# Performance work log

Hardware: AMD Instinct MI355X
Metric: run time of the kernel (lower is better)

## Reference

```python
import jax, jax.numpy as jnp
import numpy as np

B, C1, C2, H, W = 4, 96, 96, 40, 40
DE, DI, R, N, K, E, TOPK = 192, 192, 6, 16, 4, 4, 2
EPS_BN = 1e-5
EPS_LN = 1e-5


def conv1x1(x, w):
    # x: (B,C,H,W), w: (O,C)
    return jnp.einsum('bchw,oc->bohw', x, w)


def dwconv3(x, w, b):
    # depthwise 3x3, w: (C,1,3,3)
    C = x.shape[1]
    y = jax.lax.conv_general_dilated(x, w, (1, 1), 'SAME',
                                     dimension_numbers=('NCHW', 'OIHW', 'NCHW'),
                                     feature_group_count=C)
    return y + b[None, :, None, None]


def bn_eval(x, g, b):
    # BatchNorm2d in eval mode with running_mean=0, running_var=1
    s = g / jnp.sqrt(1.0 + EPS_BN)
    return x * s[None, :, None, None] + b[None, :, None, None]


def layernorm(x, g, b):
    m = x.mean(-1, keepdims=True)
    xc = x - m
    v = (xc * xc).mean(-1, keepdims=True)
    return xc / jnp.sqrt(v + EPS_LN) * g + b


def gelu(x):
    return jax.nn.gelu(x, approximate=False)


def selective_scan(xs, dts, As, Bs, Cs):
    # xs, dts: (B,K,D,L); As: (K,D,N); Bs, Cs: (B,K,N,L)
    Bb, Kk, Dd, L = xs.shape
    Nn = As.shape[-1]
    xs_l = jnp.moveaxis(xs, -1, 0)   # (L,B,K,D)
    dts_l = jnp.moveaxis(dts, -1, 0)
    Bs_l = jnp.moveaxis(Bs, -1, 0)   # (L,B,K,N)
    Cs_l = jnp.moveaxis(Cs, -1, 0)
    h0 = jnp.zeros((Bb, Kk, Dd, Nn), xs.dtype)

    def step(h, inp):
        x_t, dt_t, B_t, C_t = inp
        dA = jnp.exp(dt_t[..., None] * As)                  # (B,K,D,N)
        h = h * dA + (dt_t * x_t)[..., None] * B_t[:, :, None, :]
        y = jnp.einsum('bkdn,bkn->bkd', h, C_t)
        return h, y

    _, ys = jax.lax.scan(step, h0, (xs_l, dts_l, Bs_l, Cs_l))
    return jnp.moveaxis(ys, 0, -1)   # (B,K,D,L)


def ss2d(x, in_proj_w, conv_w, conv_b, x_proj_w, dt_w, dt_b, A_logs, Ds,
         onorm_g, onorm_b, out_proj_w):
    # x: (B, C2, H, W)
    xz = conv1x1(x, in_proj_w)                      # (B, 2*DE, H, W)
    xx, z = jnp.split(xz, 2, axis=1)
    z1 = gelu(z)
    xx = gelu(dwconv3(xx, conv_w, conv_b))          # (B, DE, H, W)

    Bb, Dd, Hh, Ww = xx.shape
    L = Hh * Ww
    x_hw = xx.reshape(Bb, Dd, L)
    x_wh = xx.transpose(0, 1, 3, 2).reshape(Bb, Dd, L)
    xs = jnp.stack([x_hw, x_wh, x_hw[..., ::-1], x_wh[..., ::-1]], axis=1)  # (B,K,D,L)

    x_dbl = jnp.einsum('bkdl,kcd->bkcl', xs, x_proj_w)
    dts_r = x_dbl[:, :, :R]
    Bs = x_dbl[:, :, R:R + N]
    Cs = x_dbl[:, :, R + N:]
    dts = jnp.einsum('bkrl,kdr->bkdl', dts_r, dt_w)
    dts = jax.nn.softplus(dts + dt_b[None, :, :, None])
    As = -jnp.exp(A_logs.reshape(K, Dd, N))

    ys = selective_scan(xs, dts, As, Bs, Cs)
    ys = ys + Ds.reshape(K, Dd)[None, :, :, None] * xs

    # CrossMerge
    y = ys[:, 0] + ys[:, 2, :, ::-1]
    y_wh = ys[:, 1] + ys[:, 3, :, ::-1]
    y = y + y_wh.reshape(Bb, Dd, Ww, Hh).transpose(0, 1, 3, 2).reshape(Bb, Dd, L)

    y = layernorm(y.transpose(0, 2, 1), onorm_g, onorm_b)   # (B,L,D)
    y = y.reshape(Bb, Hh, Ww, Dd).transpose(0, 3, 1, 2)     # (B,D,H,W)
    y = y * z1
    return conv1x1(y, out_proj_w)


def moe(x, router_w, router_b, dw_w, dw_b, pw_w, pw_b):
    Bb = x.shape[0]
    g = x.mean(axis=(2, 3))                                 # (B,C)
    logits = g @ router_w.T + router_b
    prob = jax.nn.softmax(logits / 2.0, axis=-1)
    tp, ti = jax.lax.top_k(prob, TOPK)
    tp = tp / tp.sum(-1, keepdims=True)
    wmat = jnp.zeros((Bb, E), x.dtype).at[jnp.arange(Bb)[:, None], ti].add(tp)
    out = jnp.zeros_like(x)
    for e in range(E):
        h = gelu(dwconv3(x, dw_w[e], dw_b[e]))
        h = conv1x1(h, pw_w[e]) + pw_b[e][None, :, None, None]
        out = out + wmat[:, e][:, None, None, None] * h
    return out


def _forward(x, proj_w, bn0_g, bn0_b, ls_fc1_w, ls_fc1_b, ls_bn_g, ls_bn_b,
             ls_fc2_w, ls_fc2_b, ls_fc3_w, ls_fc3_b, n1_g, n1_b,
             in_proj_w, conv_w, conv_b, x_proj_w, dt_w, dt_b, A_logs, Ds,
             onorm_g, onorm_b, out_proj_w, n2_g, n2_b,
             router_w, router_b, moe_dw_w, moe_dw_b, moe_pw_w, moe_pw_b):
    x = jax.nn.silu(bn_eval(conv1x1(x, proj_w), bn0_g, bn0_b))
    res1 = x
    # LSBlock
    h = dwconv3(x, ls_fc1_w, ls_fc1_b)
    h = bn_eval(h, ls_bn_g, ls_bn_b)
    h = conv1x1(h, ls_fc2_w) + ls_fc2_b[None, :, None, None]
    h = gelu(h)
    h = conv1x1(h, ls_fc3_w) + ls_fc3_b[None, :, None, None]
    x1 = x + h
    x1 = ss2d(bn_eval(x1, n1_g, n1_b), in_proj_w, conv_w, conv_b, x_proj_w,
              dt_w, dt_b, A_logs, Ds, onorm_g, onorm_b, out_proj_w)
    x = res1 + x1
    x2 = moe(bn_eval(x, n2_g, n2_b), router_w, router_b,
             moe_dw_w, moe_dw_b, moe_pw_w, moe_pw_b)
    return x + x2


def setup_inputs() -> dict:
    key = jax.random.key(0)
    ks = jax.random.split(key, 16)
    rn = lambda k, shape, s: jax.random.normal(k, shape, jnp.float32) * s
    ones = lambda *s: jnp.ones(s, jnp.float32)
    zeros = lambda *s: jnp.zeros(s, jnp.float32)
    return {
        'x': jax.random.normal(ks[0], (B, C1, H, W), jnp.float32),
        'proj_w': rn(ks[1], (C2, C1), 0.1),
        'bn0_g': ones(C2), 'bn0_b': zeros(C2),
        'ls_fc1_w': rn(ks[2], (C2, 1, 3, 3), 0.2), 'ls_fc1_b': zeros(C2),
        'ls_bn_g': ones(C2), 'ls_bn_b': zeros(C2),
        'ls_fc2_w': rn(ks[3], (C2, C2), 0.1), 'ls_fc2_b': zeros(C2),
        'ls_fc3_w': rn(ks[4], (C2, C2), 0.1), 'ls_fc3_b': zeros(C2),
        'n1_g': ones(C2), 'n1_b': zeros(C2),
        'in_proj_w': rn(ks[5], (2 * DE, C2), 0.1),
        'conv_w': rn(ks[6], (DE, 1, 3, 3), 0.2), 'conv_b': zeros(DE),
        'x_proj_w': rn(ks[7], (K, R + 2 * N, DI), 0.1),
        'dt_w': rn(ks[8], (K, DI, R), 0.3),
        'dt_b': rn(ks[9], (K, DI), 0.5),
        'A_logs': rn(ks[10], (K * DI, N), 0.5),
        'Ds': ones(K * DI),
        'onorm_g': ones(DI), 'onorm_b': zeros(DI),
        'out_proj_w': rn(ks[11], (C2, DE), 0.1),
        'n2_g': ones(C2), 'n2_b': zeros(C2),
        'router_w': rn(ks[12], (E, C2), 0.1), 'router_b': zeros(E),
        'moe_dw_w': rn(ks[13], (E, C2, 1, 3, 3), 0.2), 'moe_dw_b': zeros(E, C2),
        'moe_pw_w': rn(ks[14], (E, C2, C2), 0.1), 'moe_pw_b': zeros(E, C2),
    }


def reference(x, proj_w, bn0_g, bn0_b, ls_fc1_w, ls_fc1_b, ls_bn_g, ls_bn_b,
              ls_fc2_w, ls_fc2_b, ls_fc3_w, ls_fc3_b, n1_g, n1_b,
              in_proj_w, conv_w, conv_b, x_proj_w, dt_w, dt_b, A_logs, Ds,
              onorm_g, onorm_b, out_proj_w, n2_g, n2_b,
              router_w, router_b, moe_dw_w, moe_dw_b, moe_pw_w, moe_pw_b):
    return _forward(x, proj_w, bn0_g, bn0_b, ls_fc1_w, ls_fc1_b, ls_bn_g, ls_bn_b,
                    ls_fc2_w, ls_fc2_b, ls_fc3_w, ls_fc3_b, n1_g, n1_b,
                    in_proj_w, conv_w, conv_b, x_proj_w, dt_w, dt_b, A_logs, Ds,
                    onorm_g, onorm_b, out_proj_w, n2_g, n2_b,
                    router_w, router_b, moe_dw_w, moe_dw_b, moe_pw_w, moe_pw_b)
```

## Files before the change

kernel.cpp:

```cpp
#include <hip/hip_runtime.h>
#include <hip/hip_bf16.h>
#include <math.h>

#define BB 4
#define CC 96
#define LL 1600
#define DD 192
#define KK 4
#define RR 6
#define NN 16
#define EE 4
#define NCH 40
#define CLEN 40

typedef __hip_bfloat16 bf16;

__device__ __forceinline__ float geluf(float x){ return 0.5f*x*(1.0f+erff(x*0.70710678118654752440f)); }
__device__ __forceinline__ float softplusf(float x){ return (x>20.0f)? x : __logf(1.0f+__expf(x)); }
#define BNS rsqrtf(1.0f + 1e-5f)
#define LOG2E 1.44269504088896340736f

__device__ __forceinline__ int xpos(int k, int l){
  if (k==0) return l;
  if (k==2) return LL-1-l;
  int t = (k==1)? l : (LL-1-l);
  return (t%40)*40 + t/40;
}

struct P33 { const void* p[33]; };
#define NTOT 790660
__device__ const int g_cum[34] = {
  0, 614400, 623616, 623712, 623808, 624672, 624768, 624864, 624960,
  634176, 634272, 643488, 643584, 643680, 643776, 680640, 682368, 682560,
  711744, 716352, 717120, 729408, 730176, 730368, 730560, 748992, 749088,
  749184, 749568, 749572, 753028, 753412, 790276, 790660
};

__global__ void k_convert(P33 ps, float* cv){
  bool f32 = (((const unsigned*)ps.p[21])[0] == 0x3F800000u);
  int idx = blockIdx.x*256 + threadIdx.x;
  if (idx >= NTOT) return;
  int lo=0, hi=33;
  while (lo+1<hi){ int mid=(lo+hi)>>1; if (idx >= g_cum[mid]) lo=mid; else hi=mid; }
  int local = idx - g_cum[lo];
  float v = f32 ? ((const float*)ps.p[lo])[local]
                : __bfloat162float(((const bf16*)ps.p[lo])[local]);
  cv[idx] = v;
}

__global__ void k_proj(const float* x, const float* w, const float* g, const float* b_, float* out){
  __shared__ float lx[96*64];
  int bid = blockIdx.x;
  int ot = bid%3, lt = (bid/3)%25, b = bid/75;
  int l0 = lt*64, ob = ot*32;
  const float* inb = x + b*CC*LL;
  for (int i=threadIdx.x; i<96*64; i+=256) lx[i] = inb[(i>>6)*LL + l0 + (i&63)];
  __syncthreads();
  int oq = threadIdx.x>>5, lq = threadIdx.x&31;
  float acc[4][2] = {};
  #pragma unroll 4
  for (int c=0;c<96;c++){
    float x0 = lx[c*64+lq], x1 = lx[c*64+lq+32];
    #pragma unroll
    for (int jo=0;jo<4;jo++){
      float wv = w[(ob+oq+8*jo)*CC + c];
      acc[jo][0] += wv*x0; acc[jo][1] += wv*x1;
    }
  }
  #pragma unroll
  for (int jo=0;jo<4;jo++){
    int o = ob+oq+8*jo;
    float sc = g[o]*BNS, bb = b_[o];
    #pragma unroll
    for (int jl=0;jl<2;jl++){
      float v = acc[jo][jl]*sc + bb;
      out[(b*CC+o)*LL + l0+lq+32*jl] = v/(1.0f+__expf(-v));
    }
  }
}

__global__ void k_fc_gelu(const float* in, const float* w, const float* bias, float* out){
  __shared__ float lx[96*64];
  int bid = blockIdx.x;
  int ot = bid%3, lt = (bid/3)%25, b = bid/75;
  int l0 = lt*64, ob = ot*32;
  const float* inb = in + b*CC*LL;
  for (int i=threadIdx.x; i<96*64; i+=256) lx[i] = inb[(i>>6)*LL + l0 + (i&63)];
  __syncthreads();
  int oq = threadIdx.x>>5, lq = threadIdx.x&31;
  float acc[4][2] = {};
  #pragma unroll 4
  for (int c=0;c<96;c++){
    float x0 = lx[c*64+lq], x1 = lx[c*64+lq+32];
    #pragma unroll
    for (int jo=0;jo<4;jo++){
      float wv = w[(ob+oq+8*jo)*CC + c];
      acc[jo][0] += wv*x0; acc[jo][1] += wv*x1;
    }
  }
  #pragma unroll
  for (int jo=0;jo<4;jo++){
    int o = ob+oq+8*jo;
    float bb = bias[o];
    out[(b*CC+o)*LL + l0+lq]    = geluf(acc[jo][0]+bb);
    out[(b*CC+o)*LL + l0+lq+32] = geluf(acc[jo][1]+bb);
  }
}

__global__ void k_fc_res_bn(const float* in, const float* w, const float* bias, const float* res,
                            const float* g, const float* b_, float* out){
  __shared__ float lx[96*64];
  int bid = blockIdx.x;
  int ot = bid%3, lt = (bid/3)%25, b = bid/75;
  int l0 = lt*64, ob = ot*32;
  const float* inb = in + b*CC*LL;
  for (int i=threadIdx.x; i<96*64; i+=256) lx[i] = inb[(i>>6)*LL + l0 + (i&63)];
  __syncthreads();
  int oq = threadIdx.x>>5, lq = threadIdx.x&31;
  float acc[4][2] = {};
  #pragma unroll 4
  for (int c=0;c<96;c++){
    float x0 = lx[c*64+lq], x1 = lx[c*64+lq+32];
    #pragma unroll
    for (int jo=0;jo<4;jo++){
      float wv = w[(ob+oq+8*jo)*CC + c];
      acc[jo][0] += wv*x0; acc[jo][1] += wv*x1;
    }
  }
  #pragma unroll
  for (int jo=0;jo<4;jo++){
    int o = ob+oq+8*jo;
    float bb = bias[o], sc = g[o]*BNS, b2 = b_[o];
    #pragma unroll
    for (int jl=0;jl<2;jl++){
      int pos = (b*CC+o)*LL + l0+lq+32*jl;
      float v = acc[jo][jl] + bb + res[pos];
      out[pos] = v*sc + b2;
    }
  }
}

__global__ void k_inproj(const float* in, const float* w, float* xxp, float* z1){
  __shared__ float lx[96*64];
  int bid = blockIdx.x;
  int ot = bid%12, lt = (bid/12)%25, b = bid/300;
  int l0 = lt*64, ob = ot*32;
  const float* inb = in + b*CC*LL;
  for (int i=threadIdx.x; i<96*64; i+=256) lx[i] = inb[(i>>6)*LL + l0 + (i&63)];
  __syncthreads();
  int oq = threadIdx.x>>5, lq = threadIdx.x&31;
  float acc[4][2] = {};
  #pragma unroll 4
  for (int c=0;c<96;c++){
    float x0 = lx[c*64+lq], x1 = lx[c*64+lq+32];
    #pragma unroll
    for (int jo=0;jo<4;jo++){
      float wv = w[(ob+oq+8*jo)*CC + c];
      acc[jo][0] += wv*x0; acc[jo][1] += wv*x1;
    }
  }
  if (ot < 6){
    #pragma unroll
    for (int jo=0;jo<4;jo++){
      int oc = ob+oq+8*jo;
      xxp[(b*DD+oc)*LL + l0+lq]    = acc[jo][0];
      xxp[(b*DD+oc)*LL + l0+lq+32] = acc[jo][1];
    }
  } else {
    __syncthreads();
    #pragma unroll
    for (int jo=0;jo<4;jo++){
      int oo = oq+8*jo;
      lx[lq*33 + oo]      = geluf(acc[jo][0]);
      lx[(lq+32)*33 + oo] = geluf(acc[jo][1]);
    }
    __syncthreads();
    int zb = ob - 192;
    for (int i=threadIdx.x; i<64*32; i+=256){
      int u = i>>5, oo = i&31;
      z1[(b*LL + l0+u)*DD + zb + oo] = lx[u*33 + oo];
    }
  }
}

__global__ void k_ssconv(const float* in, const float* w, const float* bias, float* out){
  int idx = blockIdx.x*256 + threadIdx.x;
  if (idx >= BB*DD*LL) return;
  int l = idx%LL, d = (idx/LL)%DD, b = idx/(LL*DD);
  int y = l/40, x0 = l%40;
  const float* ip = in + (b*DD+d)*LL;
  float acc = 0.f;
  #pragma unroll
  for (int ky=0;ky<3;ky++){
    int yy = y+ky-1; if (yy<0||yy>=40) continue;
    #pragma unroll
    for (int kx=0;kx<3;kx++){
      int xx = x0+kx-1; if (xx<0||xx>=40) continue;
      acc += w[d*9+ky*3+kx] * ip[yy*40+xx];
    }
  }
  out[idx] = geluf(acc + bias[d]);
}

__global__ void k_dwbn(const float* in, const float* w, const float* bias, const float* g, const float* b_, float* out){
  int idx = blockIdx.x*256 + threadIdx.x;
  if (idx >= BB*CC*LL) return;
  int l = idx%LL, c = (idx/LL)%CC, b = idx/(LL*CC);
  int y = l/40, x0 = l%40;
  const float* ip = in + (b*CC+c)*LL;
  float acc = 0.f;
  #pragma unroll
  for (int ky=0;ky<3;ky++){
    int yy = y+ky-1; if (yy<0||yy>=40) continue;
    #pragma unroll
    for (int kx=0;kx<3;kx++){
      int xx = x0+kx-1; if (xx<0||xx>=40) continue;
      acc += w[c*9+ky*3+kx] * ip[yy*40+xx];
    }
  }
  acc += bias[c];
  out[idx] = acc*(g[c]*BNS) + b_[c];
}

__global__ void k_xs(const float* xx, float* xs){
  __shared__ float t[32][33];
  int bid = blockIdx.x;
  int lt = bid % 50, dt = (bid/50)%6, b = bid/300;
  int l0 = lt*32, d0 = dt*32;
  int tx = threadIdx.x & 31, ty = threadIdx.x >> 5;
  #pragma unroll
  for (int j=0;j<4;j++){
    int dd = ty + 8*j;
    t[dd][tx] = xx[(b*DD + d0+dd)*LL + l0 + tx];
  }
  __syncthreads();
  #pragma unroll
  for (int j=0;j<4;j++){
    int ll = ty + 8*j;
    int l = l0 + ll;
    float v = t[tx][ll];
    int lw = (l%40)*40 + l/40;
    xs[((b*2+0)*LL + l )*DD + d0 + tx] = v;
    xs[((b*2+1)*LL + lw)*DD + d0 + tx] = v;
  }
}

__global__ void k_xw(const float* xx, float* xw1, float* Y){
  __shared__ float sm[40*41];
  int bd = blockIdx.x;
  const float* ip = xx + bd*LL;
  float* op = xw1 + bd*LL;
  for (int i=threadIdx.x; i<LL; i+=256) sm[(i/40)*41 + (i%40)] = ip[i];
  float* yz0 = Y + bd*LL;
  for (int i=threadIdx.x; i<LL; i+=256) yz0[i] = 0.f;
  __syncthreads();
  for (int i=threadIdx.x; i<LL; i+=256) op[i] = sm[(i%40)*41 + (i/40)];
}

__global__ void k_xdbl(const float* xx, const float* xw1, const float* w, float* xd){
  __shared__ float lt_[32*41];
  int bid = blockIdx.x;
  int tt = bid % 50, bk = bid / 50;
  int k = bk & 3, b = bk >> 2;
  int t0 = tt*32;
  int cg = threadIdx.x >> 5, tl = threadIdx.x & 31;
  int t = t0 + tl;
  int row = (k<2)? t : (LL-1-t);
  const float* base = ((k&1)? xw1 : xx) + b*DD*LL + row;
  const float* wp[5];
  #pragma unroll
  for (int j=0;j<5;j++){
    int c = cg + 8*j; if (c>37) c = 37;
    wp[j] = w + (k*38+c)*DD;
  }
  float acc[5] = {};
  for (int d=0; d<DD; d++){
    float xv = base[d*LL];
    #pragma unroll
    for (int j=0;j<5;j++) acc[j] += wp[j][d]*xv;
  }
  #pragma unroll
  for (int j=0;j<5;j++){
    int c = cg + 8*j;
    if (c < 38) lt_[tl*41 + c] = acc[j];
  }
  __syncthreads();
  float* ob = xd + (bk*LL + t0)*40;
  for (int i=threadIdx.x; i<32*40; i+=256){
    int tr = i/40, col = i%40;
    float v;
    if (col < 32)      v = lt_[tr*41 + col + 6];
    else if (col < 38) v = lt_[tr*41 + col - 32];
    else               v = 0.f;
    ob[i] = v;
  }
}

__global__ void k_scan1(const float* xs, const float* xd, const float* dtw, const float* dtb,
                        const float* Alog, float* Pb, float* Sb){
  __shared__ float slab[CLEN*44];
  __shared__ float ldt[64*41];
  int bid = blockIdx.x;
  int dt3 = bid % 3;
  int c   = (bid/3) % NCH;
  int bk  = bid/(3*NCH);
  int k = bk & 3, b = bk >> 2;
  int d0 = dt3*64;
  const float* xrow0 = xd + (bk*LL + c*CLEN)*40;
  for (int i=threadIdx.x; i<CLEN*40; i+=256){
    slab[(i/40)*44 + (i%40)] = xrow0[i];
  }
  __syncthreads();
  for (int i=threadIdx.x; i<64*CLEN; i+=256){
    int dd = i/CLEN, j = i%CLEN;
    int kd = k*DD + d0 + dd;
    float dtr = dtb[kd];
    #pragma unroll
    for (int q=0;q<RR;q++) dtr += dtw[kd*RR+q]*slab[j*44 + 32 + q];
    ldt[dd*41 + j] = softplusf(dtr);
  }
  __syncthreads();
  int lane = threadIdx.x & 63;
  int d16 = lane & 15, g = lane >> 4;
  int dd = (threadIdx.x>>6)*16 + d16;
  int d = d0 + dd;
  int kd = k*DD + d;
  float A2[4], P[4]={1.f,1.f,1.f,1.f}, S[4]={0.f,0.f,0.f,0.f};
  #pragma unroll
  for (int n=0;n<4;n++) A2[n] = -expf(Alog[kd*NN + g*4 + n])*LOG2E;
  const float* xsb = xs + ((b*2)+(k&1))*LL*DD;
  bool rev = (k>=2);
  int t0 = c*CLEN;
  for (int j=0;j<CLEN;j++){
    int t = t0+j;
    int row = rev? (LL-1-t) : t;
    float dt = ldt[dd*41 + j];
    float4 B4 = *(const float4*)(&slab[j*44 + g*4]);
    float xv = xsb[row*DD + d];
    float u = dt*xv;
    float Ba[4] = {B4.x,B4.y,B4.z,B4.w};
    #pragma unroll
    for (int n=0;n<4;n++){
      float dA = exp2f(dt*A2[n]);
      P[n] *= dA;
      S[n] = S[n]*dA + u*Ba[n];
    }
  }
  int off = ((bk*DD + d)*NCH + c)*NN + g*4;
  *(float4*)(Pb+off) = make_float4(P[0],P[1],P[2],P[3]);
  *(float4*)(Sb+off) = make_float4(S[0],S[1],S[2],S[3]);
}

__global__ void k_scanmid(float* Pb, const float* Sb){
  int idx = blockIdx.x*256 + threadIdx.x;
  if (idx >= BB*KK*DD*NN) return;
  int n = idx%NN, bkd = idx/NN;
  float h = 0.f;
  for (int c=0;c<NCH;c++){
    int o = (bkd*NCH + c)*NN + n;
    float p = Pb[o], s = Sb[o];
    Pb[o] = h;
    h = p*h + s;
  }
}

__global__ void k_scan2(const float* xs, const float* xd, const float* dtw, const float* dtb,
                        const float* Alog, const float* Hin, const float* Ds, float* Y){
  __shared__ float slab[CLEN*44];
  __shared__ float ldt[64*41];
  int bid = blockIdx.x;
  int dt3 = bid % 3;
  int c   = (bid/3) % NCH;
  int bk  = bid/(3*NCH);
  int k = bk & 3, b = bk >> 2;
  int d0 = dt3*64;
  const float* xrow0 = xd + (bk*LL + c*CLEN)*40;
  for (int i=threadIdx.x; i<CLEN*40; i+=256){
    slab[(i/40)*44 + (i%40)] = xrow0[i];
  }
  __syncthreads();
  for (int i=threadIdx.x; i<64*CLEN; i+=256){
    int dd = i/CLEN, j = i%CLEN;
    int kd = k*DD + d0 + dd;
    float dtr = dtb[kd];
    #pragma unroll
    for (int q=0;q<RR;q++) dtr += dtw[kd*RR+q]*slab[j*44 + 32 + q];
    ldt[dd*41 + j] = softplusf(dtr);
  }
  __syncthreads();
  int lane = threadIdx.x & 63;
  int d16 = lane & 15, g = lane >> 4;
  int dd = (threadIdx.x>>6)*16 + d16;
  int d = d0 + dd;
  int kd = k*DD + d;
  int off = ((bk*DD + d)*NCH + c)*NN + g*4;
  float4 h4 = *(const float4*)(Hin+off);
  float h[4] = {h4.x, h4.y, h4.z, h4.w};
  float A2[4];
  #pragma unroll
  for (int n=0;n<4;n++) A2[n] = -expf(Alog[kd*NN + g*4 + n])*LOG2E;
  float Dv = Ds[kd];
  const float* xsb = xs + ((b*2)+(k&1))*LL*DD;
  float* yb = Y + b*LL*DD;
  bool rev = (k>=2);
  int t0 = c*CLEN;
  for (int j=0;j<CLEN;j++){
    int t = t0+j;
    int row = rev? (LL-1-t) : t;
    float dt = ldt[dd*41 + j];
    float4 B4 = *(const float4*)(&slab[j*44 + g*4]);
    float4 C4 = *(const float4*)(&slab[j*44 + 16 + g*4]);
    float xv = xsb[row*DD + d];
    float u = dt*xv;
    float Ba[4] = {B4.x,B4.y,B4.z,B4.w};
    float Ca[4] = {C4.x,C4.y,C4.z,C4.w};
    float y = 0.f;
    #pragma unroll
    for (int n=0;n<4;n++){
      float dA = exp2f(dt*A2[n]);
      h[n] = h[n]*dA + u*Ba[n];
      y += h[n]*Ca[n];
    }
    y += __shfl_xor(y, 16, 64);
    y += __shfl_xor(y, 32, 64);
    if (g==0){
      int p = xpos(k, t);
      atomicAdd(&yb[p*DD + d], y + Dv*xv);
    }
  }
}

__global__ void k_ln(const float* Y, const float* og, const float* ob, const float* z1, float* yz){
  int r = blockIdx.x*4 + (threadIdx.x >> 6);
  int lane = threadIdx.x & 63;
  const float* yp = Y + r*DD;
  float v0 = yp[lane], v1 = yp[lane+64], v2 = yp[lane+128];
  float s = v0+v1+v2;
  #pragma unroll
  for (int off=32; off>0; off>>=1) s += __shfl_xor(s, off, 64);
  float m = s*(1.0f/DD);
  float t0=v0-m, t1=v1-m, t2=v2-m;
  float vv = t0*t0+t1*t1+t2*t2;
  #pragma unroll
  for (int off=32; off>0; off>>=1) vv += __shfl_xor(vv, off, 64);
  float rs = rsqrtf(vv*(1.0f/DD) + 1e-5f);
  #pragma unroll
  for (int i=0;i<3;i++){
    int d = lane + 64*i;
    float t = (i==0?t0:(i==1?t1:t2));
    yz[r*DD + d] = (t*rs*og[d] + ob[d]) * z1[r*DD + d];
  }
}

__global__ void k_outproj(const float* yz, const float* w, const float* res, const float* g, const float* b_,
                          float* x2, float* xb){
  __shared__ float lx[64*193];
  int bid = blockIdx.x;
  int ot = bid%3, lt = (bid/3)%25, b = bid/75;
  int l0 = lt*64, ob = ot*32;
  const float* src = yz + (b*LL + l0)*DD;
  for (int i=threadIdx.x; i<64*192; i+=256) lx[(i/192)*193 + (i%192)] = src[i];
  __syncthreads();
  int oq = threadIdx.x>>5, lq = threadIdx.x&31;
  float acc[4][2] = {};
  #pragma unroll 4
  for (int c=0;c<192;c++){
    float x0 = lx[lq*193 + c], x1 = lx[(lq+32)*193 + c];
    #pragma unroll
    for (int jo=0;jo<4;jo++){
      float wv = w[(ob+oq+8*jo)*DD + c];
      acc[jo][0] += wv*x0; acc[jo][1] += wv*x1;
    }
  }
  #pragma unroll
  for (int jo=0;jo<4;jo++){
    int o = ob+oq+8*jo;
    float sc = g[o]*BNS, b2 = b_[o];
    #pragma unroll
    for (int jl=0;jl<2;jl++){
      int pos = (b*CC+o)*LL + l0+lq+32*jl;
      float v = res[pos] + acc[jo][jl];
      x2[pos] = v;
      xb[pos] = v*sc + b2;
    }
  }
}

__global__ void k_gmean(const float* xb, float* gv){
  __shared__ float sm[4];
  int bc = blockIdx.x;
  int tid = threadIdx.x;
  const float* p = xb + bc*LL;
  float s = 0.f;
  for (int l=tid; l<LL; l+=256) s += p[l];
  #pragma unroll
  for (int off=32; off>0; off>>=1) s += __shfl_xor(s, off, 64);
  if ((tid&63)==0) sm[tid>>6] = s;
  __syncthreads();
  if (tid==0) gv[bc] = (sm[0]+sm[1]+sm[2]+sm[3])*(1.0f/LL);
}

__global__ void k_router(const float* gv, const float* rw, const float* rb, float* wm){
  int b = threadIdx.x;
  if (b >= BB) return;
  float lg[EE];
  for (int e=0;e<EE;e++){
    float a = rb[e];
    for (int c=0;c<CC;c++) a += gv[b*CC+c]*rw[e*CC+c];
    lg[e] = a*0.5f;
  }
  float mx = lg[0];
  for (int e=1;e<EE;e++) mx = fmaxf(mx, lg[e]);
  float p[EE], s = 0.f;
  for (int e=0;e<EE;e++){ p[e] = __expf(lg[e]-mx); s += p[e]; }
  for (int e=0;e<EE;e++) p[e] /= s;
  int i1 = 0;
  for (int e=1;e<EE;e++) if (p[e] > p[i1]) i1 = e;
  int i2 = -1;
  for (int e=0;e<EE;e++){ if (e==i1) continue; if (i2<0 || p[e]>p[i2]) i2 = e; }
  float tot = p[i1]+p[i2];
  for (int e=0;e<EE;e++) wm[b*EE+e] = 0.f;
  wm[b*EE+i1] = p[i1]/tot;
  wm[b*EE+i2] = p[i2]/tot;
}

__global__ void k_moedw(const float* xb, const float* dw, const float* db, const float* wm, float* he){
  int idx = blockIdx.x*256 + threadIdx.x;
  if (idx >= BB*CC*LL) return;
  int l = idx%LL, c = (idx/LL)%CC, b = idx/(LL*CC);
  int y = l/40, x0 = l%40;
  const float* ip = xb + (b*CC+c)*LL;
  float v[9];
  #pragma unroll
  for (int ky=0;ky<3;ky++){
    #pragma unroll
    for (int kx=0;kx<3;kx++){
      int yy=y+ky-1, xx=x0+kx-1;
      v[ky*3+kx] = (yy<0||yy>=40||xx<0||xx>=40)? 0.f : ip[yy*40+xx];
    }
  }
  #pragma unroll
  for (int e=0;e<EE;e++){
    float wv = wm[b*EE+e];
    if (wv == 0.f) continue;
    const float* wp = dw + (e*CC+c)*9;
    float acc = db[e*CC+c];
    #pragma unroll
    for (int q=0;q<9;q++) acc += wp[q]*v[q];
    he[((e*BB+b)*CC+c)*LL+l] = geluf(acc);
  }
}

__global__ void k_final(const float* he, const float* pw, const float* pb, const float* wm,
                        const float* x2, void* out, const void* dsraw){
  __shared__ float lx[96*64];
  bool f32 = (((const unsigned*)dsraw)[0] == 0x3F800000u);
  int bid = blockIdx.x;
  int ot = bid%3, lt = (bid/3)%25, b = bid/75;
  int l0 = lt*64, ob = ot*32;
  int oq = threadIdx.x>>5, lq = threadIdx.x&31;
  float acc[4][2] = {};
  float bias[4] = {0.f,0.f,0.f,0.f};
  for (int e=0;e<EE;e++){
    float wv = wm[b*EE+e];
    if (wv == 0.f) continue;
    __syncthreads();
    const float* hb = he + (e*BB+b)*CC*LL;
    for (int i=threadIdx.x; i<96*64; i+=256) lx[i] = hb[(i>>6)*LL + l0 + (i&63)];
    __syncthreads();
    float ae[4][2] = {};
    #pragma unroll 4
    for (int c=0;c<96;c++){
      float x0 = lx[c*64+lq], x1 = lx[c*64+lq+32];
      #pragma unroll
      for (int jo=0;jo<4;jo++){
        float wvw = pw[(e*CC+ob+oq+8*jo)*CC + c];
        ae[jo][0] += wvw*x0; ae[jo][1] += wvw*x1;
      }
    }
    #pragma unroll
    for (int jo=0;jo<4;jo++){
      acc[jo][0] += wv*ae[jo][0];
      acc[jo][1] += wv*ae[jo][1];
      bias[jo] += wv*pb[e*CC+ob+oq+8*jo];
    }
  }
  #pragma unroll
  for (int jo=0;jo<4;jo++){
    int o = ob+oq+8*jo;
    #pragma unroll
    for (int jl=0;jl<2;jl++){
      int pos = (b*CC+o)*LL + l0+lq+32*jl;
      float v = x2[pos] + acc[jo][jl] + bias[jo];
      if (f32) ((float*)out)[pos] = v;
      else     ((bf16*)out)[pos] = __float2bfloat16(v);
    }
  }
}

extern "C" void kernel_launch(void* const* d_in, const int* in_sizes, int n_in,
                              void* d_out, int out_size, void* d_ws, size_t ws_size,
                              hipStream_t stream) {
  static const int cum[34] = {
    0, 614400, 623616, 623712, 623808, 624672, 624768, 624864, 624960,
    634176, 634272, 643488, 643584, 643680, 643776, 680640, 682368, 682560,
    711744, 716352, 717120, 729408, 730176, 730368, 730560, 748992, 749088,
    749184, 749568, 749572, 753028, 753412, 790276, 790660
  };
  float* ws = (float*)d_ws;
  const float* cv[33];
  P33 ps;
  for (int i=0;i<33;i++){ ps.p[i] = d_in[i]; cv[i] = ws + cum[i]; }

  const float* c_x    = cv[0];
  const float* c_pw   = cv[1];
  const float* c_bn0g = cv[2];
  const float* c_bn0b = cv[3];
  const float* c_f1w  = cv[4];
  const float* c_f1b  = cv[5];
  const float* c_lbg  = cv[6];
  const float* c_lbb  = cv[7];
  const float* c_f2w  = cv[8];
  const float* c_f2b  = cv[9];
  const float* c_f3w  = cv[10];
  const float* c_f3b  = cv[11];
  const float* c_n1g  = cv[12];
  const float* c_n1b  = cv[13];
  const float* c_ipw  = cv[14];
  const float* c_cw   = cv[15];
  const float* c_cb   = cv[16];
  const float* c_xpw  = cv[17];
  const float* c_dtw  = cv[18];
  const float* c_dtb  = cv[19];
  const float* c_al   = cv[20];
  const float* c_ds   = cv[21];
  const float* c_ong  = cv[22];
  const float* c_onb  = cv[23];
  const float* c_opw  = cv[24];
  const float* c_n2g  = cv[25];
  const float* c_n2b  = cv[26];
  const float* c_rw   = cv[27];
  const float* c_rb   = cv[28];
  const float* c_mdw  = cv[29];
  const float* c_mdb  = cv[30];
  const float* c_mpw  = cv[31];
  const float* c_mpb  = cv[32];

  float* R   = ws +   790784;
  float* T1  = ws +  1405184;
  float* X1  = T1;
  float* X2  = T1;
  float* T2  = ws +  2019584;
  float* XB  = T2;
  float* XW1 = T1;
  float* XXP = ws +  2633984;
  float* Y   = XXP;
  float* Z1  = ws +  3862784;
  float* XX  = ws +  5091584;
  float* YZ  = XX;
  float* XS  = ws +  6320384;
  float* HE  = XS;
  float* XD  = ws +  8777984;
  float* GV  = XD;
  float* WM  = XD + 384;
  float* PB  = ws +  9801984;
  float* SB  = ws + 11768064;

  const int T = 256;
  k_convert  <<<(NTOT+T-1)/T, T, 0, stream>>>(ps, ws);
  k_proj     <<<300, T, 0, stream>>>(c_x, c_pw, c_bn0g, c_bn0b, R);
  k_dwbn     <<<(BB*CC*LL+T-1)/T, T, 0, stream>>>(R, c_f1w, c_f1b, c_lbg, c_lbb, T1);
  k_fc_gelu  <<<300, T, 0, stream>>>(T1, c_f2w, c_f2b, T2);
  k_fc_res_bn<<<300, T, 0, stream>>>(T2, c_f3w, c_f3b, R, c_n1g, c_n1b, X1);
  k_inproj   <<<1200, T, 0, stream>>>(X1, c_ipw, XXP, Z1);
  k_ssconv   <<<(BB*DD*LL+T-1)/T, T, 0, stream>>>(XXP, c_cw, c_cb, XX);
  k_xs       <<<1200, T, 0, stream>>>(XX, XS);
  k_xw       <<<BB*DD, T, 0, stream>>>(XX, XW1, Y);
  k_xdbl     <<<BB*KK*50, T, 0, stream>>>(XX, XW1, c_xpw, XD);
  k_scan1    <<<BB*KK*NCH*3, T, 0, stream>>>(XS, XD, c_dtw, c_dtb, c_al, PB, SB);
  k_scanmid  <<<(BB*KK*DD*NN+T-1)/T, T, 0, stream>>>(PB, SB);
  k_scan2    <<<BB*KK*NCH*3, T, 0, stream>>>(XS, XD, c_dtw, c_dtb, c_al, PB, c_ds, Y);
  k_ln       <<<1600, T, 0, stream>>>(Y, c_ong, c_onb, Z1, YZ);
  k_outproj  <<<300, T, 0, stream>>>(YZ, c_opw, R, c_n2g, c_n2b, X2, XB);
  k_gmean    <<<BB*CC, T, 0, stream>>>(XB, GV);
  k_router   <<<1, 64, 0, stream>>>(GV, c_rw, c_rb, WM);
  k_moedw    <<<(BB*CC*LL+T-1)/T, T, 0, stream>>>(XB, c_mdw, c_mdb, WM, HE);
  k_final    <<<300, T, 0, stream>>>(HE, c_mpw, c_mpb, WM, X2, d_out, d_in[21]);
}
```

Measured before the change: 400.7 us.

## Merge transpose kernels, fold gmean/router into outproj/final, stage dt weights in LDS

```diff
diff --git a/kernel.cpp b/kernel.cpp
--- a/kernel.cpp
+++ b/kernel.cpp
@@ -222,39 +222,39 @@
   out[idx] = acc*(g[c]*BNS) + b_[c];
 }
 
-__global__ void k_xs(const float* xx, float* xs){
-  __shared__ float t[32][33];
-  int bid = blockIdx.x;
-  int lt = bid % 50, dt = (bid/50)%6, b = bid/300;
-  int l0 = lt*32, d0 = dt*32;
-  int tx = threadIdx.x & 31, ty = threadIdx.x >> 5;
-  #pragma unroll
-  for (int j=0;j<4;j++){
-    int dd = ty + 8*j;
-    t[dd][tx] = xx[(b*DD + d0+dd)*LL + l0 + tx];
-  }
-  __syncthreads();
-  #pragma unroll
-  for (int j=0;j<4;j++){
-    int ll = ty + 8*j;
-    int l = l0 + ll;
-    float v = t[tx][ll];
-    int lw = (l%40)*40 + l/40;
-    xs[((b*2+0)*LL + l )*DD + d0 + tx] = v;
-    xs[((b*2+1)*LL + lw)*DD + d0 + tx] = v;
-  }
-}
-
-__global__ void k_xw(const float* xx, float* xw1, float* Y){
+__global__ void k_xsxw(const float* xx, float* xs, float* xw1, float* Y){
   __shared__ float sm[40*41];
-  int bd = blockIdx.x;
-  const float* ip = xx + bd*LL;
-  float* op = xw1 + bd*LL;
-  for (int i=threadIdx.x; i<LL; i+=256) sm[(i/40)*41 + (i%40)] = ip[i];
-  float* yz0 = Y + bd*LL;
-  for (int i=threadIdx.x; i<LL; i+=256) yz0[i] = 0.f;
-  __syncthreads();
-  for (int i=threadIdx.x; i<LL; i+=256) op[i] = sm[(i%40)*41 + (i/40)];
+  int bid = blockIdx.x;
+  if (bid < 1200){
+    float (*t)[33] = (float(*)[33])sm;
+    int lt = bid % 50, dt = (bid/50)%6, b = bid/300;
+    int l0 = lt*32, d0 = dt*32;
+    int tx = threadIdx.x & 31, ty = threadIdx.x >> 5;
+    #pragma unroll
+    for (int j=0;j<4;j++){
+      int dd = ty + 8*j;
+      t[dd][tx] = xx[(b*DD + d0+dd)*LL + l0 + tx];
+    }
+    __syncthreads();
+    #pragma unroll
+    for (int j=0;j<4;j++){
+      int ll = ty + 8*j;
+      int l = l0 + ll;
+      float v = t[tx][ll];
+      int lw = (l%40)*40 + l/40;
+      xs[((b*2+0)*LL + l )*DD + d0 + tx] = v;
+      xs[((b*2+1)*LL + lw)*DD + d0 + tx] = v;
+    }
+  } else {
+    int bd = bid - 1200;
+    const float* ip = xx + bd*LL;
+    float* op = xw1 + bd*LL;
+    for (int i=threadIdx.x; i<LL; i+=256) sm[(i/40)*41 + (i%40)] = ip[i];
+    float* yz0 = Y + bd*LL;
+    for (int i=threadIdx.x; i<LL; i+=256) yz0[i] = 0.f;
+    __syncthreads();
+    for (int i=threadIdx.x; i<LL; i+=256) op[i] = sm[(i%40)*41 + (i/40)];
+  }
 }
 
 __global__ void k_xdbl(const float* xx, const float* xw1, const float* w, float* xd){
@@ -300,6 +300,8 @@
                         const float* Alog, float* Pb, float* Sb){
   __shared__ float slab[CLEN*44];
   __shared__ float ldt[64*41];
+  __shared__ float ldtw[64*7];
+  __shared__ float ldtb[64];
   int bid = blockIdx.x;
   int dt3 = bid % 3;
   int c   = (bid/3) % NCH;
@@ -307,17 +309,18 @@
   int k = bk & 3, b = bk >> 2;
   int d0 = dt3*64;
   const float* xrow0 = xd + (bk*LL + c*CLEN)*40;
-  for (int i=threadIdx.x; i<CLEN*40; i+=256){
+  for (int i=threadIdx.x; i<CLEN*40; i+=256)
     slab[(i/40)*44 + (i%40)] = xrow0[i];
-  }
+  for (int i=threadIdx.x; i<64*RR; i+=256)
+    ldtw[(i/RR)*7 + (i%RR)] = dtw[(k*DD+d0 + i/RR)*RR + (i%RR)];
+  if (threadIdx.x < 64) ldtb[threadIdx.x] = dtb[k*DD+d0+threadIdx.x];
   __syncthreads();
   for (int i=threadIdx.x; i<64*CLEN; i+=256){
-    int dd = i/CLEN, j = i%CLEN;
-    int kd = k*DD + d0 + dd;
-    float dtr = dtb[kd];
-    #pragma unroll
-    for (int q=0;q<RR;q++) dtr += dtw[kd*RR+q]*slab[j*44 + 32 + q];
-    ldt[dd*41 + j] = softplusf(dtr);
+    int j = i>>6, dd = i&63;
+    float dtr = ldtb[dd];
+    #pragma unroll
+    for (int q=0;q<RR;q++) dtr += ldtw[dd*7+q]*slab[j*44+32+q];
+    ldt[dd*41+j] = softplusf(dtr);
   }
   __syncthreads();
   int lane = threadIdx.x & 63;
@@ -368,6 +371,8 @@
                         const float* Alog, const float* Hin, const float* Ds, float* Y){
   __shared__ float slab[CLEN*44];
   __shared__ float ldt[64*41];
+  __shared__ float ldtw[64*7];
+  __shared__ float ldtb[64];
   int bid = blockIdx.x;
   int dt3 = bid % 3;
   int c   = (bid/3) % NCH;
@@ -375,17 +380,18 @@
   int k = bk & 3, b = bk >> 2;
   int d0 = dt3*64;
   const float* xrow0 = xd + (bk*LL + c*CLEN)*40;
-  for (int i=threadIdx.x; i<CLEN*40; i+=256){
+  for (int i=threadIdx.x; i<CLEN*40; i+=256)
     slab[(i/40)*44 + (i%40)] = xrow0[i];
-  }
+  for (int i=threadIdx.x; i<64*RR; i+=256)
+    ldtw[(i/RR)*7 + (i%RR)] = dtw[(k*DD+d0 + i/RR)*RR + (i%RR)];
+  if (threadIdx.x < 64) ldtb[threadIdx.x] = dtb[k*DD+d0+threadIdx.x];
   __syncthreads();
   for (int i=threadIdx.x; i<64*CLEN; i+=256){
-    int dd = i/CLEN, j = i%CLEN;
-    int kd = k*DD + d0 + dd;
-    float dtr = dtb[kd];
-    #pragma unroll
-    for (int q=0;q<RR;q++) dtr += dtw[kd*RR+q]*slab[j*44 + 32 + q];
-    ldt[dd*41 + j] = softplusf(dtr);
+    int j = i>>6, dd = i&63;
+    float dtr = ldtb[dd];
+    #pragma unroll
+    for (int q=0;q<RR;q++) dtr += ldtw[dd*7+q]*slab[j*44+32+q];
+    ldt[dd*41+j] = softplusf(dtr);
   }
   __syncthreads();
   int lane = threadIdx.x & 63;
@@ -430,7 +436,10 @@
   }
 }
 
-__global__ void k_ln(const float* Y, const float* og, const float* ob, const float* z1, float* yz){
+__global__ void k_ln(const float* Y, const float* og, const float* ob, const float* z1, float* yz, float* gv){
+  if (blockIdx.x == 0){
+    for (int i=threadIdx.x; i<BB*CC; i+=256) gv[i] = 0.f;
+  }
   int r = blockIdx.x*4 + (threadIdx.x >> 6);
   int lane = threadIdx.x & 63;
   const float* yp = Y + r*DD;
@@ -453,7 +462,7 @@
 }
 
 __global__ void k_outproj(const float* yz, const float* w, const float* res, const float* g, const float* b_,
-                          float* x2, float* xb){
+                          float* x2, float* xb, float* gv){
   __shared__ float lx[64*193];
   int bid = blockIdx.x;
   int ot = bid%3, lt = (bid/3)%25, b = bid/75;
@@ -476,55 +485,23 @@
   for (int jo=0;jo<4;jo++){
     int o = ob+oq+8*jo;
     float sc = g[o]*BNS, b2 = b_[o];
-    #pragma unroll
-    for (int jl=0;jl<2;jl++){
-      int pos = (b*CC+o)*LL + l0+lq+32*jl;
-      float v = res[pos] + acc[jo][jl];
-      x2[pos] = v;
-      xb[pos] = v*sc + b2;
-    }
-  }
-}
-
-__global__ void k_gmean(const float* xb, float* gv){
-  __shared__ float sm[4];
-  int bc = blockIdx.x;
-  int tid = threadIdx.x;
-  const float* p = xb + bc*LL;
-  float s = 0.f;
-  for (int l=tid; l<LL; l+=256) s += p[l];
-  #pragma unroll
-  for (int off=32; off>0; off>>=1) s += __shfl_xor(s, off, 64);
-  if ((tid&63)==0) sm[tid>>6] = s;
-  __syncthreads();
-  if (tid==0) gv[bc] = (sm[0]+sm[1]+sm[2]+sm[3])*(1.0f/LL);
-}
-
-__global__ void k_router(const float* gv, const float* rw, const float* rb, float* wm){
-  int b = threadIdx.x;
-  if (b >= BB) return;
-  float lg[EE];
-  for (int e=0;e<EE;e++){
-    float a = rb[e];
-    for (int c=0;c<CC;c++) a += gv[b*CC+c]*rw[e*CC+c];
-    lg[e] = a*0.5f;
-  }
-  float mx = lg[0];
-  for (int e=1;e<EE;e++) mx = fmaxf(mx, lg[e]);
-  float p[EE], s = 0.f;
-  for (int e=0;e<EE;e++){ p[e] = __expf(lg[e]-mx); s += p[e]; }
-  for (int e=0;e<EE;e++) p[e] /= s;
-  int i1 = 0;
-  for (int e=1;e<EE;e++) if (p[e] > p[i1]) i1 = e;
-  int i2 = -1;
-  for (int e=0;e<EE;e++){ if (e==i1) continue; if (i2<0 || p[e]>p[i2]) i2 = e; }
-  float tot = p[i1]+p[i2];
-  for (int e=0;e<EE;e++) wm[b*EE+e] = 0.f;
-  wm[b*EE+i1] = p[i1]/tot;
-  wm[b*EE+i2] = p[i2]/tot;
-}
-
-__global__ void k_moedw(const float* xb, const float* dw, const float* db, const float* wm, float* he){
+    float xb0 = 0.f, xb1 = 0.f;
+    {
+      int pos = (b*CC+o)*LL + l0+lq;
+      float v = res[pos] + acc[jo][0];
+      x2[pos] = v; xb0 = v*sc + b2; xb[pos] = xb0;
+      pos += 32;
+      float v2 = res[pos] + acc[jo][1];
+      x2[pos] = v2; xb1 = v2*sc + b2; xb[pos] = xb1;
+    }
+    float sv = xb0 + xb1;
+    #pragma unroll
+    for (int off=1; off<32; off<<=1) sv += __shfl_xor(sv, off, 64);
+    if (lq == 0) atomicAdd(&gv[b*CC + o], sv*(1.0f/LL));
+  }
+}
+
+__global__ void k_moedw(const float* xb, const float* dw, const float* db, float* he){
   int idx = blockIdx.x*256 + threadIdx.x;
   if (idx >= BB*CC*LL) return;
   int l = idx%LL, c = (idx/LL)%CC, b = idx/(LL*CC);
@@ -541,8 +518,6 @@
   }
   #pragma unroll
   for (int e=0;e<EE;e++){
-    float wv = wm[b*EE+e];
-    if (wv == 0.f) continue;
     const float* wp = dw + (e*CC+c)*9;
     float acc = db[e*CC+c];
     #pragma unroll
@@ -551,18 +526,41 @@
   }
 }
 
-__global__ void k_final(const float* he, const float* pw, const float* pb, const float* wm,
+__global__ void k_final(const float* he, const float* pw, const float* pb,
+                        const float* gv, const float* rw, const float* rb,
                         const float* x2, void* out, const void* dsraw){
   __shared__ float lx[96*64];
   bool f32 = (((const unsigned*)dsraw)[0] == 0x3F800000u);
   int bid = blockIdx.x;
   int ot = bid%3, lt = (bid/3)%25, b = bid/75;
   int l0 = lt*64, ob = ot*32;
+  float wmv[EE];
+  {
+    float lg[EE];
+    for (int e=0;e<EE;e++){
+      float a = rb[e];
+      for (int cc2=0;cc2<CC;cc2++) a += gv[b*CC+cc2]*rw[e*CC+cc2];
+      lg[e] = a*0.5f;
+    }
+    float mx = lg[0];
+    for (int e=1;e<EE;e++) mx = fmaxf(mx, lg[e]);
+    float p[EE], s = 0.f;
+    for (int e=0;e<EE;e++){ p[e] = __expf(lg[e]-mx); s += p[e]; }
+    for (int e=0;e<EE;e++) p[e] /= s;
+    int i1 = 0;
+    for (int e=1;e<EE;e++) if (p[e] > p[i1]) i1 = e;
+    int i2 = -1;
+    for (int e=0;e<EE;e++){ if (e==i1) continue; if (i2<0 || p[e]>p[i2]) i2 = e; }
+    float tot = p[i1]+p[i2];
+    for (int e=0;e<EE;e++) wmv[e] = 0.f;
+    wmv[i1] = p[i1]/tot;
+    wmv[i2] = p[i2]/tot;
+  }
   int oq = threadIdx.x>>5, lq = threadIdx.x&31;
   float acc[4][2] = {};
   float bias[4] = {0.f,0.f,0.f,0.f};
   for (int e=0;e<EE;e++){
-    float wv = wm[b*EE+e];
+    float wv = wmv[e];
     if (wv == 0.f) continue;
     __syncthreads();
     const float* hb = he + (e*BB+b)*CC*LL;
@@ -662,7 +660,6 @@
   float* HE  = XS;
   float* XD  = ws +  8777984;
   float* GV  = XD;
-  float* WM  = XD + 384;
   float* PB  = ws +  9801984;
   float* SB  = ws + 11768064;
 
@@ -674,16 +671,13 @@
   k_fc_res_bn<<<300, T, 0, stream>>>(T2, c_f3w, c_f3b, R, c_n1g, c_n1b, X1);
   k_inproj   <<<1200, T, 0, stream>>>(X1, c_ipw, XXP, Z1);
   k_ssconv   <<<(BB*DD*LL+T-1)/T, T, 0, stream>>>(XXP, c_cw, c_cb, XX);
-  k_xs       <<<1200, T, 0, stream>>>(XX, XS);
-  k_xw       <<<BB*DD, T, 0, stream>>>(XX, XW1, Y);
+  k_xsxw     <<<1968, T, 0, stream>>>(XX, XS, XW1, Y);
   k_xdbl     <<<BB*KK*50, T, 0, stream>>>(XX, XW1, c_xpw, XD);
   k_scan1    <<<BB*KK*NCH*3, T, 0, stream>>>(XS, XD, c_dtw, c_dtb, c_al, PB, SB);
   k_scanmid  <<<(BB*KK*DD*NN+T-1)/T, T, 0, stream>>>(PB, SB);
   k_scan2    <<<BB*KK*NCH*3, T, 0, stream>>>(XS, XD, c_dtw, c_dtb, c_al, PB, c_ds, Y);
-  k_ln       <<<1600, T, 0, stream>>>(Y, c_ong, c_onb, Z1, YZ);
-  k_outproj  <<<300, T, 0, stream>>>(YZ, c_opw, R, c_n2g, c_n2b, X2, XB);
-  k_gmean    <<<BB*CC, T, 0, stream>>>(XB, GV);
-  k_router   <<<1, 64, 0, stream>>>(GV, c_rw, c_rb, WM);
-  k_moedw    <<<(BB*CC*LL+T-1)/T, T, 0, stream>>>(XB, c_mdw, c_mdb, WM, HE);
-  k_final    <<<300, T, 0, stream>>>(HE, c_mpw, c_mpb, WM, X2, d_out, d_in[21]);
-}
+  k_ln       <<<1600, T, 0, stream>>>(Y, c_ong, c_onb, Z1, YZ, GV);
+  k_outproj  <<<300, T, 0, stream>>>(YZ, c_opw, R, c_n2g, c_n2b, X2, XB, GV);
+  k_moedw    <<<(BB*CC*LL+T-1)/T, T, 0, stream>>>(XB, c_mdw, c_mdb, HE);
+  k_final    <<<300, T, 0, stream>>>(HE, c_mpw, c_mpb, GV, c_rw, c_rb, X2, d_out, d_in[21]);
+}
```

After: 393.5 us. Within noise of the previous version (-1.8%).
